# Optimization experiments

Hardware: AMD Instinct MI355X
Metric: run time of the kernel (lower is better)

Reference implementation:

```python
import jax, jax.numpy as jnp
import numpy as np

B, D, H = 32768, 688, 4
DH = D // H          # 172 head dim (d_model // h, overrides ctor d_k)
MH = 128             # mlp hidden
EPS = 1e-5
SCALE = 1.0 / float(np.sqrt(DH))


def _ln(x, g, b):
    m = jnp.mean(x, -1, keepdims=True)
    v = jnp.var(x, -1, keepdims=True)  # biased var, matches torch LayerNorm
    return (x - m) / jnp.sqrt(v + EPS) * g + b


def setup_inputs() -> dict:
    key = jax.random.key(0)
    ks = jax.random.split(key, 16)
    w = lambda k, o, i: jax.random.normal(k, (o, i), jnp.float32) * 0.001  # init.normal_(std=0.001)
    z = lambda n: jnp.zeros((n,), jnp.float32)
    o = lambda n: jnp.ones((n,), jnp.float32)
    return dict(
        x=jax.random.normal(ks[0], (B, D), jnp.float32),
        x2=jax.random.normal(ks[1], (B, D), jnp.float32),
        Wq_v=w(ks[2], D, D), bq_v=z(D),
        Wk_v=w(ks[3], D, D), bk_v=z(D),
        Wv_v=w(ks[4], D, D), bv_v=z(D),
        Wq_i=w(ks[5], D, D), bq_i=z(D),
        Wk_i=w(ks[6], D, D), bk_i=z(D),
        Wv_i=w(ks[7], D, D), bv_i=z(D),
        Wo_v=w(ks[8], D, D), bo_v=z(D),
        Wo_i=w(ks[9], D, D), bo_i=z(D),
        ln1_g=o(D), ln1_b=z(D), ln2_g=o(D), ln2_b=z(D),
        ln3_g=o(D), ln3_b=z(D), ln4_g=o(D), ln4_b=z(D),
        m1v_W=w(ks[10], MH, D), m1v_b=z(MH),
        m2v_W=w(ks[11], D, MH), m2v_b=z(D),
        m1i_W=w(ks[12], MH, D), m1i_b=z(MH),
        m2i_W=w(ks[13], D, MH), m2i_b=z(D),
        coef=o(8),  # LearnableCoefficient 1..8, all init to 1.0
    )


def reference(x, x2,
              Wq_v, bq_v, Wk_v, bk_v, Wv_v, bv_v,
              Wq_i, bq_i, Wk_i, bk_i, Wv_i, bv_i,
              Wo_v, bo_v, Wo_i, bo_i,
              ln1_g, ln1_b, ln2_g, ln2_b, ln3_g, ln3_b, ln4_g, ln4_b,
              m1v_W, m1v_b, m2v_W, m2v_b, m1i_W, m1i_b, m2i_W, m2i_b,
              coef):
    rgb = _ln(x, ln1_g, ln1_b)
    ir = _ln(x2, ln2_g, ln2_b)
    proj = lambda t, W, b: (t @ W.T + b).reshape(-1, H, DH)  # (B, h, d_k)
    q_vis, k_vis, v_vis = proj(rgb, Wq_v, bq_v), proj(rgb, Wk_v, bk_v), proj(rgb, Wv_v, bv_v)
    q_ir, k_ir, v_ir = proj(ir, Wq_i, bq_i), proj(ir, Wk_i, bk_i), proj(ir, Wv_i, bv_i)
    # cross attention over heads: scores are (B, h, h)
    att_vis = jax.nn.softmax(jnp.einsum('bhd,bgd->bhg', q_ir, k_vis) * SCALE, -1)
    att_ir = jax.nn.softmax(jnp.einsum('bhd,bgd->bhg', q_vis, k_ir) * SCALE, -1)
    out_vis = jnp.einsum('bhg,bgd->bhd', att_vis, v_vis).reshape(-1, D) @ Wo_v.T + bo_v
    out_ir = jnp.einsum('bhg,bgd->bhd', att_ir, v_ir).reshape(-1, D) @ Wo_i.T + bo_i
    out_vis = coef[0] * x + coef[1] * out_vis
    out_ir = coef[2] * x2 + coef[3] * out_ir
    mv = jax.nn.gelu(_ln(out_vis, ln3_g, ln3_b) @ m1v_W.T + m1v_b, approximate=False) @ m2v_W.T + m2v_b
    mi = jax.nn.gelu(_ln(out_ir, ln4_g, ln4_b) @ m1i_W.T + m1i_b, approximate=False) @ m2i_W.T + m2i_b
    out_vis = coef[4] * out_vis + coef[5] * mv
    out_ir = coef[6] * out_ir + coef[7] * mi
    return out_vis, out_ir
```

## Files before the change

kernel.cpp:

```cpp
#include <hip/hip_runtime.h>
#include <cmath>


#define B_ROWS 32768
#define D_DIM  688
#define DP     704
#define DH_DIM 172
#define MH_DIM 128

typedef unsigned short ushort_t;
typedef __attribute__((ext_vector_type(8))) __bf16 bf16x8;
typedef __attribute__((ext_vector_type(4))) float  f32x4;

__device__ __forceinline__ float b2f(ushort_t u) {
    return __builtin_bit_cast(float, (unsigned int)u << 16);
}
__device__ __forceinline__ ushort_t f2bf(float f) {
    unsigned int u = __builtin_bit_cast(unsigned int, f);
    u += 0x7FFFu + ((u >> 16) & 1u);
    return (ushort_t)(u >> 16);
}

__device__ __forceinline__ void gl2lds16(const ushort_t* g, ushort_t* l) {
    __builtin_amdgcn_global_load_lds(
        (const __attribute__((address_space(1))) unsigned int*)g,
        (__attribute__((address_space(3))) unsigned int*)l, 16, 0, 0);
}

struct CvtJobs {
    const float* src[12];
    ushort_t*    dst[12];
    int O[12], Opad[12], Kin[12], Kpad[12];
    int bstart[13];
};

__global__ __launch_bounds__(256)
void cvt_all(CvtJobs jobs)
{
    int b = blockIdx.x;
    int j = 0;
    while (b >= jobs.bstart[j + 1]) ++j;
    const int t = (b - jobs.bstart[j]) * 256 + threadIdx.x;
    const int Kpad = jobs.Kpad[j];
    const int Kin  = jobs.Kin[j];
    const int cpr  = Kpad >> 3;
    if (t >= jobs.Opad[j] * cpr) return;
    const int o = t / cpr;
    const int c = t - o * cpr;
    unsigned int p0 = 0, p1 = 0, p2 = 0, p3 = 0;
    if (o < jobs.O[j] && (c * 8 + 8) <= Kin) {
        const float* s = jobs.src[j] + (size_t)o * Kin + c * 8;
        float4 f0 = reinterpret_cast<const float4*>(s)[0];
        float4 f1 = reinterpret_cast<const float4*>(s)[1];
        p0 = f2bf(f0.x) | ((unsigned int)f2bf(f0.y) << 16);
        p1 = f2bf(f0.z) | ((unsigned int)f2bf(f0.w) << 16);
        p2 = f2bf(f1.x) | ((unsigned int)f2bf(f1.y) << 16);
        p3 = f2bf(f1.z) | ((unsigned int)f2bf(f1.w) << 16);
    }
    *reinterpret_cast<uint4*>(jobs.dst[j] + (size_t)o * Kpad + c * 8) =
        make_uint4(p0, p1, p2, p3);
}

__global__ __launch_bounds__(256)
void pack_bias(const float* __restrict__ a0, const float* __restrict__ a1,
               const float* __restrict__ a2, const float* __restrict__ b0,
               const float* __restrict__ b1, const float* __restrict__ b2,
               float* __restrict__ dv, float* __restrict__ di)
{
    int t = blockIdx.x * 256 + threadIdx.x;
    if (t >= 2064) return;
    float v, w;
    if (t < 688)       { v = a0[t];        w = b0[t]; }
    else if (t < 1376) { v = a1[t - 688];  w = b1[t - 688]; }
    else               { v = a2[t - 1376]; w = b2[t - 1376]; }
    dv[t] = v; di[t] = w;
}

__global__ __launch_bounds__(256)
void ln_kernel(const float* __restrict__ Xv, const float* __restrict__ Xi,
               const float* __restrict__ gv, const float* __restrict__ bv,
               const float* __restrict__ gi, const float* __restrict__ bi,
               ushort_t* __restrict__ Yv, ushort_t* __restrict__ Yi)
{
    const int lane = threadIdx.x & 63;
    const int wave = threadIdx.x >> 6;
    const long w = (long)blockIdx.x * 4 + wave;
    const float* X; const float* g; const float* b; ushort_t* Y; long r;
    if (w < B_ROWS) { X = Xv; g = gv; b = bv; Y = Yv; r = w; }
    else            { X = Xi; g = gi; b = bi; Y = Yi; r = w - B_ROWS; }

    const float4* row = reinterpret_cast<const float4*>(X + r * D_DIM);
    float4 v0 = row[lane];
    float4 v1 = row[lane + 64];
    float4 v2 = make_float4(0.f, 0.f, 0.f, 0.f);
    if (lane < 44) v2 = row[lane + 128];

    float s  = v0.x + v0.y + v0.z + v0.w + v1.x + v1.y + v1.z + v1.w
             + v2.x + v2.y + v2.z + v2.w;
    float s2 = v0.x*v0.x + v0.y*v0.y + v0.z*v0.z + v0.w*v0.w
             + v1.x*v1.x + v1.y*v1.y + v1.z*v1.z + v1.w*v1.w
             + v2.x*v2.x + v2.y*v2.y + v2.z*v2.z + v2.w*v2.w;
#pragma unroll
    for (int m = 32; m; m >>= 1) { s += __shfl_xor(s, m); s2 += __shfl_xor(s2, m); }

    const float mean = s * (1.f / 688.f);
    const float var  = s2 * (1.f / 688.f) - mean * mean;
    const float rstd = rsqrtf(var + 1e-5f);

    const float4* g4 = reinterpret_cast<const float4*>(g);
    const float4* b4 = reinterpret_cast<const float4*>(b);
    ushort4* out4 = reinterpret_cast<ushort4*>(Y + r * DP);

    {
        float4 gg = g4[lane], bb = b4[lane];
        ushort4 o;
        o.x = f2bf((v0.x - mean) * rstd * gg.x + bb.x);
        o.y = f2bf((v0.y - mean) * rstd * gg.y + bb.y);
        o.z = f2bf((v0.z - mean) * rstd * gg.z + bb.z);
        o.w = f2bf((v0.w - mean) * rstd * gg.w + bb.w);
        out4[lane] = o;
    }
    {
        float4 gg = g4[lane + 64], bb = b4[lane + 64];
        ushort4 o;
        o.x = f2bf((v1.x - mean) * rstd * gg.x + bb.x);
        o.y = f2bf((v1.y - mean) * rstd * gg.y + bb.y);
        o.z = f2bf((v1.z - mean) * rstd * gg.z + bb.z);
        o.w = f2bf((v1.w - mean) * rstd * gg.w + bb.w);
        out4[lane + 64] = o;
    }
    if (lane < 44) {
        float4 gg = g4[lane + 128], bb = b4[lane + 128];
        ushort4 o;
        o.x = f2bf((v2.x - mean) * rstd * gg.x + bb.x);
        o.y = f2bf((v2.y - mean) * rstd * gg.y + bb.y);
        o.z = f2bf((v2.z - mean) * rstd * gg.z + bb.z);
        o.w = f2bf((v2.w - mean) * rstd * gg.w + bb.w);
        out4[lane + 128] = o;
    } else if (lane < 48) {
        out4[lane + 128] = make_ushort4(0, 0, 0, 0);
    }
}

template<int MODE>
__global__ __launch_bounds__(512, 1)
void gemm8(const ushort_t* __restrict__ A0, const ushort_t* __restrict__ A1,
           const ushort_t* __restrict__ W0, const ushort_t* __restrict__ W1,
           const float* __restrict__ bias0, const float* __restrict__ bias1,
           ushort_t* __restrict__ out0, ushort_t* __restrict__ out1,
           const float* __restrict__ res0, const float* __restrict__ res1,
           const float* __restrict__ coef, int ca0, int cb0, int ca1, int cb1,
           int NBn, int N, int K, int lda, int ldw, int ldo)
{
    __shared__ __align__(16) ushort_t lds8[65536];

    const int q8 = gridDim.x >> 3;
    const int v  = (blockIdx.x & 7) * q8 + (blockIdx.x >> 3);
    const int nb = v % NBn;
    const int tmp = v / NBn;
    const int mb = tmp & 127;
    const int zz = tmp >> 7;

    const ushort_t* A = zz ? A1 : A0;
    const ushort_t* W = zz ? W1 : W0;
    const float* bias = zz ? bias1 : bias0;
    ushort_t* outp    = zz ? out1 : out0;
    const float* resid = zz ? res1 : res0;
    const int ca = zz ? ca1 : ca0;
    const int cb = zz ? cb1 : cb0;

    const int tid  = threadIdx.x;
    const int lane = tid & 63;
    const int wave = tid >> 6;
    const int wrow = wave >> 2;
    const int wcol = wave & 3;
    const int m0 = mb * 256;
    const int n0 = nb * 256;
    const int rl16 = lane & 15;
    const int q4   = lane >> 4;

    const int r0 = tid >> 3;
    const int u0 = tid & 7;
    const int swz0 = ((u0 ^ (r0 & 7)) * 8);

    f32x4 acc[8][4];
#pragma unroll
    for (int i = 0; i < 8; ++i)
#pragma unroll
        for (int j = 0; j < 4; ++j)
            acc[i][j] = f32x4{0.f, 0.f, 0.f, 0.f};

    const int NT = K >> 6;

#define STAGE8(mat, rbase, ld, kt, hf, tilebase) do {                              \
    const ushort_t* _s = (mat) + (size_t)((rbase) + (hf)*128 + r0) * (ld)          \
                         + (kt)*64 + swz0;                                         \
    gl2lds16(_s,                 (tilebase) + (hf)*8192 + wave*512);               \
    gl2lds16(_s + 64*(size_t)(ld), (tilebase) + (hf)*8192 + 4096 + wave*512);      \
} while (0)

#define RD_A(base, mib, kkv) do {                                                  \
    _Pragma("unroll")                                                              \
    for (int i = 0; i < 4; ++i) {                                                  \
        const int row_ = wrow*128 + ((mib)+i)*16 + rl16;                           \
        const int un_  = (((kkv) >> 3) + q4) ^ (lane & 7);                         \
        af[i] = *reinterpret_cast<const bf16x8*>((base) + row_*64 + un_*8);        \
    } } while (0)

#define RD_B(base, kkv) do {                                                       \
    _Pragma("unroll")                                                              \
    for (int j = 0; j < 4; ++j) {                                                  \
        const int row_ = wcol*64 + j*16 + rl16;                                    \
        const int un_  = (((kkv) >> 3) + q4) ^ (lane & 7);                         \
        bw[j] = *reinterpret_cast<const bf16x8*>((base) + row_*64 + un_*8);        \
    } } while (0)

#define MFMA16(mib) do {                                                           \
    __builtin_amdgcn_s_setprio(1);                                                 \
    _Pragma("unroll")                                                              \
    for (int i = 0; i < 4; ++i)                                                    \
    _Pragma("unroll")                                                              \
    for (int j = 0; j < 4; ++j)                                                    \
        acc[(mib)+i][j] =                                                          \
            __builtin_amdgcn_mfma_f32_16x16x32_bf16(af[i], bw[j], acc[(mib)+i][j], \
                                                    0, 0, 0);                      \
    __builtin_amdgcn_s_setprio(0);                                                 \
} while (0)

    STAGE8(A, m0, lda, 0, 0, lds8);
    STAGE8(A, m0, lda, 0, 1, lds8);
    STAGE8(W, n0, ldw, 0, 0, lds8 + 32768);
    STAGE8(W, n0, ldw, 0, 1, lds8 + 32768);
    STAGE8(W, n0, ldw, 1, 0, lds8 + 49152);
    asm volatile("s_waitcnt vmcnt(2)" ::: "memory");
    __builtin_amdgcn_s_barrier();

    for (int t = 0; t < NT; ++t) {
        ushort_t* const Ab  = lds8 + ((t & 1) * 16384);
        ushort_t* const Bb  = lds8 + 32768 + ((t & 1) * 16384);
        ushort_t* const An  = lds8 + (((t + 1) & 1) * 16384);
        ushort_t* const Bn1 = lds8 + 32768 + (((t + 1) & 1) * 16384);
        ushort_t* const Bn2 = Bb;
        const int tn1 = (t + 1 < NT) ? t + 1 : NT - 1;
        const int tn2 = (t + 2 < NT) ? t + 2 : NT - 1;

        bf16x8 af[4], bw[4];

        RD_A(Ab, 0, 0);
        RD_B(Bb, 0);
        STAGE8(A, m0, lda, tn1, 0, An);
        STAGE8(W, n0, ldw, tn1, 1, Bn1);
        __builtin_amdgcn_s_barrier();
        MFMA16(0);
        __builtin_amdgcn_s_barrier();

        RD_A(Ab, 4, 0);
        STAGE8(A, m0, lda, tn1, 1, An);
        __builtin_amdgcn_s_barrier();
        MFMA16(4);
        __builtin_amdgcn_s_barrier();

        RD_A(Ab, 0, 32);
        RD_B(Bb, 32);
        __builtin_amdgcn_s_barrier();
        MFMA16(0);
        __builtin_amdgcn_s_barrier();

        RD_A(Ab, 4, 32);
        STAGE8(W, n0, ldw, tn2, 0, Bn2);
        asm volatile("s_waitcnt vmcnt(2)" ::: "memory");
        __builtin_amdgcn_s_barrier();
        MFMA16(4);
        __builtin_amdgcn_s_barrier();
    }

    asm volatile("s_waitcnt vmcnt(0)" ::: "memory");
    __builtin_amdgcn_s_barrier();

    ushort_t* const Cl = lds8;
#pragma unroll
    for (int mi = 0; mi < 8; ++mi)
#pragma unroll
        for (int nj = 0; nj < 4; ++nj)
#pragma unroll
            for (int r = 0; r < 4; ++r) {
                const int row  = wrow*128 + mi*16 + q4*4 + r;
                const int colL = wcol*64 + nj*16 + rl16;
                const int blk  = (colL >> 3) ^ (((row >> 2) & 3) << 1);
                Cl[row*256 + blk*8 + (colL & 7)] = f2bf(acc[mi][nj][r]);
            }
    __syncthreads();

    float cA = 0.f, cB = 1.f;
    if constexpr (MODE == 1) { cA = coef[ca]; cB = coef[cb]; }
#pragma unroll
    for (int it2 = 0; it2 < 16; ++it2) {
        const int c   = it2 * 512 + tid;
        const int row = c >> 5;
        const int lb  = c & 31;
        const int gcol = n0 + lb * 8;
        if (gcol >= N) continue;
        const int pb = lb ^ (((row >> 2) & 3) << 1);
        uint4 pv = *reinterpret_cast<const uint4*>(Cl + row*256 + pb*8);
        const ushort_t* pu = (const ushort_t*)&pv;
        float4 b0 = *reinterpret_cast<const float4*>(bias + gcol);
        float4 b1 = *reinterpret_cast<const float4*>(bias + gcol + 4);
        const float bb[8] = {b0.x, b0.y, b0.z, b0.w, b1.x, b1.y, b1.z, b1.w};
        const size_t idx = (size_t)(m0 + row) * ldo + gcol;
        ushort_t o[8];
        if constexpr (MODE == 0) {
#pragma unroll
            for (int k = 0; k < 8; ++k) o[k] = f2bf(b2f(pu[k]) + bb[k]);
        } else {
            const float* rp = resid + idx;
            float4 r0_ = reinterpret_cast<const float4*>(rp)[0];
            float4 r1_ = reinterpret_cast<const float4*>(rp)[1];
            const float rr[8] = {r0_.x, r0_.y, r0_.z, r0_.w, r1_.x, r1_.y, r1_.z, r1_.w};
#pragma unroll
            for (int k = 0; k < 8; ++k)
                o[k] = f2bf(cA * rr[k] + cB * (b2f(pu[k]) + bb[k]));
        }
        *reinterpret_cast<uint4*>(outp + idx) = *reinterpret_cast<uint4*>(o);
    }
#undef STAGE8
#undef RD_A
#undef RD_B
#undef MFMA16
}

__global__ __launch_bounds__(256)
void mlp_fused(const ushort_t* __restrict__ ov0, const ushort_t* __restrict__ ov1,
               const float* __restrict__ g0, const float* __restrict__ b0,
               const float* __restrict__ g1, const float* __restrict__ b1,
               const ushort_t* __restrict__ W10, const ushort_t* __restrict__ W11,
               const float* __restrict__ mb10, const float* __restrict__ mb11,
               const ushort_t* __restrict__ W20, const ushort_t* __restrict__ W21,
               const float* __restrict__ mb20, const float* __restrict__ mb21,
               const float* __restrict__ coef,
               float* __restrict__ out0, float* __restrict__ out1)
{
    __shared__ __align__(16) ushort_t hraw[32 * 712];
    __shared__ __align__(16) ushort_t gbuf[32 * 136];
    __shared__ float glds[704];
    __shared__ float blds[704];
    __shared__ float mlds[32];
    __shared__ float rlds[32];

    const int zz = blockIdx.y;
    const ushort_t* ovb = zz ? ov1 : ov0;
    const float* lg = zz ? g1 : g0;
    const float* lb = zz ? b1 : b0;
    const ushort_t* W1 = zz ? W11 : W10;
    const float* mb1 = zz ? mb11 : mb10;
    const ushort_t* W2 = zz ? W21 : W20;
    const float* mb2 = zz ? mb21 : mb20;
    float* outp = zz ? out1 : out0;
    const float cA = coef[zz ? 6 : 4];
    const float cB = coef[zz ? 7 : 5];

    const int tid  = threadIdx.x;
    const int lane = tid & 63;
    const int wv   = tid >> 6;
    const long r0  = (long)blockIdx.x * 32;

    if (tid < 176) {
        float4 gg = make_float4(0, 0, 0, 0), bb = make_float4(0, 0, 0, 0);
        if (tid < 172) {
            gg = reinterpret_cast<const float4*>(lg)[tid];
            bb = reinterpret_cast<const float4*>(lb)[tid];
        }
        reinterpret_cast<float4*>(glds)[tid] = gg;
        reinterpret_cast<float4*>(blds)[tid] = bb;
    }

#pragma unroll
    for (int it = 0; it < 11; ++it) {
        const int c = it * 256 + tid;
        const int row = c / 88;
        const int u = c - row * 88;
        uint4 vv = make_uint4(0, 0, 0, 0);
        if (u < 86)
            vv = *reinterpret_cast<const uint4*>(ovb + (r0 + row) * 688 + u * 8);
        *reinterpret_cast<uint4*>(&hraw[row * 712 + u * 8]) = vv;
    }
    __syncthreads();

    for (int rr = 0; rr < 8; ++rr) {
        const int row = wv * 8 + rr;
        const ushort_t* hp = &hraw[row * 712];
        ushort4 a0 = *reinterpret_cast<const ushort4*>(hp + lane * 4);
        ushort4 a1 = *reinterpret_cast<const ushort4*>(hp + 256 + lane * 4);
        ushort4 a2 = make_ushort4(0, 0, 0, 0);
        if (lane < 44) a2 = *reinterpret_cast<const ushort4*>(hp + 512 + lane * 4);
        float e[12] = {b2f(a0.x), b2f(a0.y), b2f(a0.z), b2f(a0.w),
                       b2f(a1.x), b2f(a1.y), b2f(a1.z), b2f(a1.w),
                       b2f(a2.x), b2f(a2.y), b2f(a2.z), b2f(a2.w)};
        float s = 0.f, s2 = 0.f;
#pragma unroll
        for (int k = 0; k < 12; ++k) { s += e[k]; s2 += e[k] * e[k]; }
#pragma unroll
        for (int m = 32; m; m >>= 1) { s += __shfl_xor(s, m); s2 += __shfl_xor(s2, m); }
        if (lane == 0) {
            const float mean = s * (1.f / 688.f);
            const float var  = s2 * (1.f / 688.f) - mean * mean;
            mlds[row] = mean;
            rlds[row] = rsqrtf(var + 1e-5f);
        }
    }
    __syncthreads();

#pragma unroll
    for (int it = 0; it < 11; ++it) {
        const int c = it * 256 + tid;
        if (c < 2752) {
            const int row = c / 86;
            const int u = c - row * 86;
            uint4 vv = *reinterpret_cast<const uint4*>(&hraw[row * 712 + u * 8]);
            const float mean = mlds[row], rstd = rlds[row];
            const ushort_t* pe = (const ushort_t*)&vv;
            ushort_t o[8];
#pragma unroll
            for (int k = 0; k < 8; ++k)
                o[k] = f2bf((b2f(pe[k]) - mean) * rstd * glds[u * 8 + k] + blds[u * 8 + k]);
            *reinterpret_cast<uint4*>(&hraw[row * 712 + u * 8]) = *reinterpret_cast<uint4*>(o);
        }
    }
    __syncthreads();

    const int rl16 = lane & 15;
    const int q4   = lane >> 4;

    {
        f32x4 acc[2][2];
#pragma unroll
        for (int i = 0; i < 2; ++i) { acc[i][0] = f32x4{0,0,0,0}; acc[i][1] = f32x4{0,0,0,0}; }
        for (int kt = 0; kt < 11; ++kt) {
#pragma unroll
            for (int kk = 0; kk < 64; kk += 32) {
                bf16x8 af[2], bw[2];
#pragma unroll
                for (int n = 0; n < 2; ++n)
                    bw[n] = *reinterpret_cast<const bf16x8*>(
                        W1 + (size_t)(wv * 32 + n * 16 + rl16) * 704 + kt * 64 + kk + q4 * 8);
#pragma unroll
                for (int i = 0; i < 2; ++i)
                    af[i] = *reinterpret_cast<const bf16x8*>(
                        &hraw[(i * 16 + rl16) * 712 + kt * 64 + kk + q4 * 8]);
#pragma unroll
                for (int i = 0; i < 2; ++i)
#pragma unroll
                    for (int n = 0; n < 2; ++n)
                        acc[i][n] = __builtin_amdgcn_mfma_f32_16x16x32_bf16(
                            af[i], bw[n], acc[i][n], 0, 0, 0);
            }
        }
        const int rb = q4 * 4;
#pragma unroll
        for (int n = 0; n < 2; ++n) {
            const int col = wv * 32 + n * 16 + rl16;
            const float bc = mb1[col];
#pragma unroll
            for (int i = 0; i < 2; ++i)
#pragma unroll
                for (int r = 0; r < 4; ++r) {
                    float val = acc[i][n][r] + bc;
                    val = 0.5f * val * (1.0f + erff(val * 0.70710678118654752f));
                    gbuf[(i * 16 + rb + r) * 136 + col] = f2bf(val);
                }
        }
    }
    __syncthreads();

    for (int ch = 0; ch < 11; ++ch) {
        const int col16 = wv * 176 + ch * 16;
        if (col16 >= 688) continue;
        f32x4 acc2[2];
        acc2[0] = f32x4{0, 0, 0, 0};
        acc2[1] = f32x4{0, 0, 0, 0};
#pragma unroll
        for (int kk = 0; kk < 4; ++kk) {
            bf16x8 bw2 = *reinterpret_cast<const bf16x8*>(
                W2 + (size_t)(col16 + rl16) * 128 + kk * 32 + q4 * 8);
            bf16x8 af2[2];
#pragma unroll
            for (int i = 0; i < 2; ++i)
                af2[i] = *reinterpret_cast<const bf16x8*>(
                    &gbuf[(i * 16 + rl16) * 136 + kk * 32 + q4 * 8]);
#pragma unroll
            for (int i = 0; i < 2; ++i)
                acc2[i] = __builtin_amdgcn_mfma_f32_16x16x32_bf16(af2[i], bw2, acc2[i], 0, 0, 0);
        }
        const int col = col16 + rl16;
        const float bc = mb2[col];
#pragma unroll
        for (int i = 0; i < 2; ++i)
#pragma unroll
            for (int r = 0; r < 4; ++r) {
                const long row = r0 + i * 16 + q4 * 4 + r;
                const float raw = b2f(ovb[row * 688 + col]);
                outp[row * 688 + col] = cA * raw + cB * (acc2[i][r] + bc);
            }
    }
}

__global__ __launch_bounds__(256)
void attn_kernel(const ushort_t* __restrict__ qkv_v, const ushort_t* __restrict__ qkv_i,
                 ushort_t* __restrict__ ctx_v, ushort_t* __restrict__ ctx_i)
{
    const int lane = threadIdx.x & 63;
    const int wave = threadIdx.x >> 6;
    const long r = (long)blockIdx.x * 4 + wave;
    const ushort_t* bv = qkv_v + r * 2064;
    const ushort_t* bi = qkv_i + r * 2064;

    float sv[4][4], si[4][4];
#pragma unroll
    for (int h = 0; h < 4; ++h)
#pragma unroll
        for (int g = 0; g < 4; ++g) { sv[h][g] = 0.f; si[h][g] = 0.f; }

    float vvr[3][4], vir[3][4];
#pragma unroll
    for (int it = 0; it < 3; ++it) {
        const int d = lane + it * 64;
        const bool ok = d < DH_DIM;
        float qv[4], kv[4], qi[4], ki[4];
#pragma unroll
        for (int h = 0; h < 4; ++h) {
            const int o = h * DH_DIM + d;
            qv[h]      = ok ? b2f(bv[o]) : 0.f;
            kv[h]      = ok ? b2f(bv[D_DIM + o]) : 0.f;
            vvr[it][h] = ok ? b2f(bv[2 * D_DIM + o]) : 0.f;
            qi[h]      = ok ? b2f(bi[o]) : 0.f;
            ki[h]      = ok ? b2f(bi[D_DIM + o]) : 0.f;
            vir[it][h] = ok ? b2f(bi[2 * D_DIM + o]) : 0.f;
        }
#pragma unroll
        for (int h = 0; h < 4; ++h)
#pragma unroll
            for (int g = 0; g < 4; ++g) {
                sv[h][g] += qi[h] * kv[g];
                si[h][g] += qv[h] * ki[g];
            }
    }

#pragma unroll
    for (int h = 0; h < 4; ++h)
#pragma unroll
        for (int g = 0; g < 4; ++g) {
            float a = sv[h][g], b = si[h][g];
#pragma unroll
            for (int m = 32; m; m >>= 1) { a += __shfl_xor(a, m); b += __shfl_xor(b, m); }
            sv[h][g] = a; si[h][g] = b;
        }

    const float scale = 0.07624928516630235f;
    float av[4][4], ai[4][4];
#pragma unroll
    for (int h = 0; h < 4; ++h) {
        float m1 = fmaxf(fmaxf(sv[h][0], sv[h][1]), fmaxf(sv[h][2], sv[h][3])) * scale;
        float m2 = fmaxf(fmaxf(si[h][0], si[h][1]), fmaxf(si[h][2], si[h][3])) * scale;
        float d1 = 0.f, d2 = 0.f;
#pragma unroll
        for (int g = 0; g < 4; ++g) {
            av[h][g] = expf(sv[h][g] * scale - m1); d1 += av[h][g];
            ai[h][g] = expf(si[h][g] * scale - m2); d2 += ai[h][g];
        }
        const float r1 = 1.f / d1, r2 = 1.f / d2;
#pragma unroll
        for (int g = 0; g < 4; ++g) { av[h][g] *= r1; ai[h][g] *= r2; }
    }

#pragma unroll
    for (int it = 0; it < 3; ++it) {
        const int d = lane + it * 64;
        if (d < DH_DIM) {
#pragma unroll
            for (int h = 0; h < 4; ++h) {
                float cv = av[h][0] * vvr[it][0] + av[h][1] * vvr[it][1]
                         + av[h][2] * vvr[it][2] + av[h][3] * vvr[it][3];
                float ci = ai[h][0] * vir[it][0] + ai[h][1] * vir[it][1]
                         + ai[h][2] * vir[it][2] + ai[h][3] * vir[it][3];
                ctx_v[r * DP + h * DH_DIM + d] = f2bf(cv);
                ctx_i[r * DP + h * DH_DIM + d] = f2bf(ci);
            }
        }
    }
    if (lane < 16) {
        ctx_v[r * DP + 688 + lane] = 0;
        ctx_i[r * DP + 688 + lane] = 0;
    }
}

extern "C" void kernel_launch(void* const* d_in, const int* in_sizes, int n_in,
                              void* d_out, int out_size, void* d_ws, size_t ws_size,
                              hipStream_t stream)
{
    if (n_in < 35) return;
    const float* x     = (const float*)d_in[0];
    const float* x2    = (const float*)d_in[1];
    const float* Wq_v  = (const float*)d_in[2];
    const float* bq_v  = (const float*)d_in[3];
    const float* Wk_v  = (const float*)d_in[4];
    const float* bk_v  = (const float*)d_in[5];
    const float* Wv_v  = (const float*)d_in[6];
    const float* bv_v  = (const float*)d_in[7];
    const float* Wq_i  = (const float*)d_in[8];
    const float* bq_i  = (const float*)d_in[9];
    const float* Wk_i  = (const float*)d_in[10];
    const float* bk_i  = (const float*)d_in[11];
    const float* Wv_i  = (const float*)d_in[12];
    const float* bv_i  = (const float*)d_in[13];
    const float* Wo_v  = (const float*)d_in[14];
    const float* bo_v  = (const float*)d_in[15];
    const float* Wo_i  = (const float*)d_in[16];
    const float* bo_i  = (const float*)d_in[17];
    const float* ln1_g = (const float*)d_in[18];
    const float* ln1_b = (const float*)d_in[19];
    const float* ln2_g = (const float*)d_in[20];
    const float* ln2_b = (const float*)d_in[21];
    const float* ln3_g = (const float*)d_in[22];
    const float* ln3_b = (const float*)d_in[23];
    const float* ln4_g = (const float*)d_in[24];
    const float* ln4_b = (const float*)d_in[25];
    const float* m1v_W = (const float*)d_in[26];
    const float* m1v_b = (const float*)d_in[27];
    const float* m2v_W = (const float*)d_in[28];
    const float* m2v_b = (const float*)d_in[29];
    const float* m1i_W = (const float*)d_in[30];
    const float* m1i_b = (const float*)d_in[31];
    const float* m2i_W = (const float*)d_in[32];
    const float* m2i_b = (const float*)d_in[33];
    const float* coef  = (const float*)d_in[34];

    const size_t BDP = (size_t)B_ROWS * DP;
    const size_t BD  = (size_t)B_ROWS * D_DIM;

    char* ws = (char*)d_ws;
    size_t off = 0;
    auto give = [&](size_t bytes) {
        char* p = ws + off;
        off += (bytes + 255) & ~(size_t)255;
        return p;
    };
    ushort_t* Wcat_v = (ushort_t*)give(2304ull * DP * 2);
    ushort_t* Wcat_i = (ushort_t*)give(2304ull * DP * 2);
    ushort_t* Wo_vb  = (ushort_t*)give(768ull * DP * 2);
    ushort_t* Wo_ib  = (ushort_t*)give(768ull * DP * 2);
    ushort_t* m1vb   = (ushort_t*)give(128ull * DP * 2);
    ushort_t* m1ib   = (ushort_t*)give(128ull * DP * 2);
    ushort_t* m2vb   = (ushort_t*)give(768ull * 128 * 2);
    ushort_t* m2ib   = (ushort_t*)give(768ull * 128 * 2);
    float*    bcat_v = (float*)give(2064 * 4);
    float*    bcat_i = (float*)give(2064 * 4);
    char* regX = give(BDP * 2 * 2);
    char* regQ = give((size_t)B_ROWS * 2064 * 2 * 2);
    if (ws_size < off) return;

    ushort_t* xn_v  = (ushort_t*)regX;
    ushort_t* xn_i  = xn_v + BDP;
    ushort_t* ctx_v = xn_v;
    ushort_t* ctx_i = xn_i;
    ushort_t* qkv_v = (ushort_t*)regQ;
    ushort_t* qkv_i = qkv_v + (size_t)B_ROWS * 2064;
    ushort_t* ovb   = (ushort_t*)regQ;
    ushort_t* oib   = ovb + BD;

    float* ov = (float*)d_out;
    float* oi = ov + BD;

    CvtJobs J;
    const float* srcs[12] = {Wq_v, Wk_v, Wv_v, Wq_i, Wk_i, Wv_i,
                             Wo_v, Wo_i, m1v_W, m1i_W, m2v_W, m2i_W};
    ushort_t* dsts[12] = {Wcat_v, Wcat_v + 688 * DP, Wcat_v + 1376 * DP,
                          Wcat_i, Wcat_i + 688 * DP, Wcat_i + 1376 * DP,
                          Wo_vb, Wo_ib, m1vb, m1ib, m2vb, m2ib};
    int Os[12]    = {688, 688, 688, 688, 688, 688, 688, 688, 128, 128, 688, 688};
    int Opads[12] = {688, 688, 928, 688, 688, 928, 768, 768, 128, 128, 768, 768};
    int Kins[12]  = {688, 688, 688, 688, 688, 688, 688, 688, 688, 688, 128, 128};
    int Kpads[12] = {DP, DP, DP, DP, DP, DP, DP, DP, DP, DP, 128, 128};
    int bs = 0;
    for (int j = 0; j < 12; ++j) {
        J.src[j] = srcs[j]; J.dst[j] = dsts[j];
        J.O[j] = Os[j]; J.Opad[j] = Opads[j]; J.Kin[j] = Kins[j]; J.Kpad[j] = Kpads[j];
        J.bstart[j] = bs;
        bs += (Opads[j] * (Kpads[j] >> 3) + 255) / 256;
    }
    J.bstart[12] = bs;
    cvt_all<<<dim3(bs), dim3(256), 0, stream>>>(J);

    pack_bias<<<dim3(9), dim3(256), 0, stream>>>(bq_v, bk_v, bv_v, bq_i, bk_i, bv_i,
                                                 bcat_v, bcat_i);

    ln_kernel<<<dim3(2 * B_ROWS / 4), dim3(256), 0, stream>>>(
        x, x2, ln1_g, ln1_b, ln2_g, ln2_b, xn_v, xn_i);

    gemm8<0><<<dim3(128 * 9 * 2), dim3(512), 0, stream>>>(
        xn_v, xn_i, Wcat_v, Wcat_i, bcat_v, bcat_i, qkv_v, qkv_i,
        nullptr, nullptr, nullptr, 0, 0, 0, 0, 9, 2064, DP, DP, DP, 2064);

    attn_kernel<<<dim3(B_ROWS / 4), dim3(256), 0, stream>>>(qkv_v, qkv_i, ctx_v, ctx_i);

    gemm8<1><<<dim3(128 * 3 * 2), dim3(512), 0, stream>>>(
        ctx_v, ctx_i, Wo_vb, Wo_ib, bo_v, bo_i, ovb, oib,
        x, x2, coef, 0, 1, 2, 3, 3, 688, DP, DP, DP, 688);

    mlp_fused<<<dim3(B_ROWS / 32, 2), dim3(256), 0, stream>>>(
        ovb, oib, ln3_g, ln3_b, ln4_g, ln4_b,
        m1vb, m1ib, m1v_b, m1i_b, m2vb, m2ib, m2v_b, m2i_b,
        coef, ov, oi);
}
```

Before: 681.6 us.

## Replace 256x256 GEMM tile with 256x128 tile and triple-buffered K=32 pipeline

Rewrites the projection GEMM kernel to use a 256x128 output tile with 8 waves in a 4x2 layout, a K step of 32, and a three-stage LDS ring (72 KB instead of 128 KB). This permits two blocks per CU. It also lowers weight padding from 928 to 800 rows, which cuts wasted N tiles on the QKV GEMM. The aim is better occupancy and less padding waste, at the cost of lower arithmetic intensity per tile and more barriers per FLOP.

```diff
diff --git a/kernel.cpp b/kernel.cpp
--- a/kernel.cpp
+++ b/kernel.cpp
@@ -143,8 +143,8 @@
 }
 
 template<int MODE>
-__global__ __launch_bounds__(512, 1)
-void gemm8(const ushort_t* __restrict__ A0, const ushort_t* __restrict__ A1,
+__global__ __launch_bounds__(512, 2)
+void gemmT(const ushort_t* __restrict__ A0, const ushort_t* __restrict__ A1,
            const ushort_t* __restrict__ W0, const ushort_t* __restrict__ W1,
            const float* __restrict__ bias0, const float* __restrict__ bias1,
            ushort_t* __restrict__ out0, ushort_t* __restrict__ out1,
@@ -152,7 +152,7 @@
            const float* __restrict__ coef, int ca0, int cb0, int ca1, int cb1,
            int NBn, int N, int K, int lda, int ldw, int ldo)
 {
-    __shared__ __align__(16) ushort_t lds8[65536];
+    __shared__ __align__(16) ushort_t lds[36864];
 
     const int q8 = gridDim.x >> 3;
     const int v  = (blockIdx.x & 7) * q8 + (blockIdx.x >> 3);
@@ -172,136 +172,97 @@
     const int tid  = threadIdx.x;
     const int lane = tid & 63;
     const int wave = tid >> 6;
-    const int wrow = wave >> 2;
-    const int wcol = wave & 3;
+    const int wrow = wave >> 1;
+    const int wcol = wave & 1;
     const int m0 = mb * 256;
-    const int n0 = nb * 256;
+    const int n0 = nb * 128;
     const int rl16 = lane & 15;
     const int q4   = lane >> 4;
 
-    const int r0 = tid >> 3;
-    const int u0 = tid & 7;
-    const int swz0 = ((u0 ^ (r0 & 7)) * 8);
-
-    f32x4 acc[8][4];
-#pragma unroll
-    for (int i = 0; i < 8; ++i)
+    const int r0a  = tid >> 2;
+    const int swzk = ((tid & 3) ^ ((tid >> 3) & 3)) * 8;
+
+    f32x4 acc[4][4];
+#pragma unroll
+    for (int i = 0; i < 4; ++i)
 #pragma unroll
         for (int j = 0; j < 4; ++j)
             acc[i][j] = f32x4{0.f, 0.f, 0.f, 0.f};
 
-    const int NT = K >> 6;
-
-#define STAGE8(mat, rbase, ld, kt, hf, tilebase) do {                              \
-    const ushort_t* _s = (mat) + (size_t)((rbase) + (hf)*128 + r0) * (ld)          \
-                         + (kt)*64 + swz0;                                         \
-    gl2lds16(_s,                 (tilebase) + (hf)*8192 + wave*512);               \
-    gl2lds16(_s + 64*(size_t)(ld), (tilebase) + (hf)*8192 + 4096 + wave*512);      \
+    const int NT = K >> 5;
+
+#define STAGET(kt, bb) do {                                                        \
+    const ushort_t* _sa = A + (size_t)(m0 + r0a) * lda + (kt)*32 + swzk;           \
+    gl2lds16(_sa,                    lds + (bb)*12288 + wave*512);                 \
+    gl2lds16(_sa + 128*(size_t)lda,  lds + (bb)*12288 + 4096 + wave*512);          \
+    const ushort_t* _sb = W + (size_t)(n0 + r0a) * ldw + (kt)*32 + swzk;           \
+    gl2lds16(_sb,                    lds + (bb)*12288 + 8192 + wave*512);          \
 } while (0)
 
-#define RD_A(base, mib, kkv) do {                                                  \
-    _Pragma("unroll")                                                              \
-    for (int i = 0; i < 4; ++i) {                                                  \
-        const int row_ = wrow*128 + ((mib)+i)*16 + rl16;                           \
-        const int un_  = (((kkv) >> 3) + q4) ^ (lane & 7);                         \
-        af[i] = *reinterpret_cast<const bf16x8*>((base) + row_*64 + un_*8);        \
-    } } while (0)
-
-#define RD_B(base, kkv) do {                                                       \
-    _Pragma("unroll")                                                              \
-    for (int j = 0; j < 4; ++j) {                                                  \
-        const int row_ = wcol*64 + j*16 + rl16;                                    \
-        const int un_  = (((kkv) >> 3) + q4) ^ (lane & 7);                         \
-        bw[j] = *reinterpret_cast<const bf16x8*>((base) + row_*64 + un_*8);        \
-    } } while (0)
-
-#define MFMA16(mib) do {                                                           \
-    __builtin_amdgcn_s_setprio(1);                                                 \
-    _Pragma("unroll")                                                              \
-    for (int i = 0; i < 4; ++i)                                                    \
-    _Pragma("unroll")                                                              \
-    for (int j = 0; j < 4; ++j)                                                    \
-        acc[(mib)+i][j] =                                                          \
-            __builtin_amdgcn_mfma_f32_16x16x32_bf16(af[i], bw[j], acc[(mib)+i][j], \
-                                                    0, 0, 0);                      \
-    __builtin_amdgcn_s_setprio(0);                                                 \
-} while (0)
-
-    STAGE8(A, m0, lda, 0, 0, lds8);
-    STAGE8(A, m0, lda, 0, 1, lds8);
-    STAGE8(W, n0, ldw, 0, 0, lds8 + 32768);
-    STAGE8(W, n0, ldw, 0, 1, lds8 + 32768);
-    STAGE8(W, n0, ldw, 1, 0, lds8 + 49152);
-    asm volatile("s_waitcnt vmcnt(2)" ::: "memory");
+    STAGET(0, 0);
+    STAGET(1, 1);
+    asm volatile("s_waitcnt vmcnt(3)" ::: "memory");
     __builtin_amdgcn_s_barrier();
 
     for (int t = 0; t < NT; ++t) {
-        ushort_t* const Ab  = lds8 + ((t & 1) * 16384);
-        ushort_t* const Bb  = lds8 + 32768 + ((t & 1) * 16384);
-        ushort_t* const An  = lds8 + (((t + 1) & 1) * 16384);
-        ushort_t* const Bn1 = lds8 + 32768 + (((t + 1) & 1) * 16384);
-        ushort_t* const Bn2 = Bb;
-        const int tn1 = (t + 1 < NT) ? t + 1 : NT - 1;
+        const int cbuf = t % 3;
+        const int pbuf = (t + 2) % 3;
         const int tn2 = (t + 2 < NT) ? t + 2 : NT - 1;
 
         bf16x8 af[4], bw[4];
-
-        RD_A(Ab, 0, 0);
-        RD_B(Bb, 0);
-        STAGE8(A, m0, lda, tn1, 0, An);
-        STAGE8(W, n0, ldw, tn1, 1, Bn1);
+#pragma unroll
+        for (int i = 0; i < 4; ++i) {
+            const int row_ = wrow * 64 + i * 16 + rl16;
+            af[i] = *reinterpret_cast<const bf16x8*>(
+                lds + cbuf * 12288 + row_ * 32 + ((q4 ^ ((row_ >> 1) & 3)) * 8));
+        }
+#pragma unroll
+        for (int j = 0; j < 4; ++j) {
+            const int row_ = wcol * 64 + j * 16 + rl16;
+            bw[j] = *reinterpret_cast<const bf16x8*>(
+                lds + cbuf * 12288 + 8192 + row_ * 32 + ((q4 ^ ((row_ >> 1) & 3)) * 8));
+        }
+        STAGET(tn2, pbuf);
+        asm volatile("s_waitcnt vmcnt(3)" ::: "memory");
         __builtin_amdgcn_s_barrier();
-        MFMA16(0);
-        __builtin_amdgcn_s_barrier();
-
-        RD_A(Ab, 4, 0);
-        STAGE8(A, m0, lda, tn1, 1, An);
-        __builtin_amdgcn_s_barrier();
-        MFMA16(4);
-        __builtin_amdgcn_s_barrier();
-
-        RD_A(Ab, 0, 32);
-        RD_B(Bb, 32);
-        __builtin_amdgcn_s_barrier();
-        MFMA16(0);
-        __builtin_amdgcn_s_barrier();
-
-        RD_A(Ab, 4, 32);
-        STAGE8(W, n0, ldw, tn2, 0, Bn2);
-        asm volatile("s_waitcnt vmcnt(2)" ::: "memory");
-        __builtin_amdgcn_s_barrier();
-        MFMA16(4);
+        __builtin_amdgcn_s_setprio(1);
+#pragma unroll
+        for (int i = 0; i < 4; ++i)
+#pragma unroll
+            for (int j = 0; j < 4; ++j)
+                acc[i][j] = __builtin_amdgcn_mfma_f32_16x16x32_bf16(af[i], bw[j], acc[i][j], 0, 0, 0);
+        __builtin_amdgcn_s_setprio(0);
         __builtin_amdgcn_s_barrier();
     }
 
     asm volatile("s_waitcnt vmcnt(0)" ::: "memory");
     __builtin_amdgcn_s_barrier();
 
-    ushort_t* const Cl = lds8;
-#pragma unroll
-    for (int mi = 0; mi < 8; ++mi)
+    ushort_t* const Cl = lds;
+#pragma unroll
+    for (int mi = 0; mi < 4; ++mi)
 #pragma unroll
         for (int nj = 0; nj < 4; ++nj)
 #pragma unroll
             for (int r = 0; r < 4; ++r) {
-                const int row  = wrow*128 + mi*16 + q4*4 + r;
-                const int colL = wcol*64 + nj*16 + rl16;
+                const int row  = wrow * 64 + mi * 16 + q4 * 4 + r;
+                const int colL = wcol * 64 + nj * 16 + rl16;
                 const int blk  = (colL >> 3) ^ (((row >> 2) & 3) << 1);
-                Cl[row*256 + blk*8 + (colL & 7)] = f2bf(acc[mi][nj][r]);
+                Cl[row * 128 + blk * 8 + (colL & 7)] = f2bf(acc[mi][nj][r]);
             }
     __syncthreads();
 
     float cA = 0.f, cB = 1.f;
     if constexpr (MODE == 1) { cA = coef[ca]; cB = coef[cb]; }
 #pragma unroll
-    for (int it2 = 0; it2 < 16; ++it2) {
+    for (int it2 = 0; it2 < 8; ++it2) {
         const int c   = it2 * 512 + tid;
-        const int row = c >> 5;
-        const int lb  = c & 31;
+        const int row = c >> 4;
+        const int lb  = c & 15;
         const int gcol = n0 + lb * 8;
         if (gcol >= N) continue;
         const int pb = lb ^ (((row >> 2) & 3) << 1);
-        uint4 pv = *reinterpret_cast<const uint4*>(Cl + row*256 + pb*8);
+        uint4 pv = *reinterpret_cast<const uint4*>(Cl + row * 128 + pb * 8);
         const ushort_t* pu = (const ushort_t*)&pv;
         float4 b0 = *reinterpret_cast<const float4*>(bias + gcol);
         float4 b1 = *reinterpret_cast<const float4*>(bias + gcol + 4);
@@ -322,10 +283,7 @@
         }
         *reinterpret_cast<uint4*>(outp + idx) = *reinterpret_cast<uint4*>(o);
     }
-#undef STAGE8
-#undef RD_A
-#undef RD_B
-#undef MFMA16
+#undef STAGET
 }
 
 __global__ __launch_bounds__(256)
@@ -676,7 +634,7 @@
                           Wcat_i, Wcat_i + 688 * DP, Wcat_i + 1376 * DP,
                           Wo_vb, Wo_ib, m1vb, m1ib, m2vb, m2ib};
     int Os[12]    = {688, 688, 688, 688, 688, 688, 688, 688, 128, 128, 688, 688};
-    int Opads[12] = {688, 688, 928, 688, 688, 928, 768, 768, 128, 128, 768, 768};
+    int Opads[12] = {688, 688, 800, 688, 688, 800, 768, 768, 128, 128, 768, 768};
     int Kins[12]  = {688, 688, 688, 688, 688, 688, 688, 688, 688, 688, 128, 128};
     int Kpads[12] = {DP, DP, DP, DP, DP, DP, DP, DP, DP, DP, 128, 128};
     int bs = 0;
@@ -695,15 +653,15 @@
     ln_kernel<<<dim3(2 * B_ROWS / 4), dim3(256), 0, stream>>>(
         x, x2, ln1_g, ln1_b, ln2_g, ln2_b, xn_v, xn_i);
 
-    gemm8<0><<<dim3(128 * 9 * 2), dim3(512), 0, stream>>>(
+    gemmT<0><<<dim3(128 * 17 * 2), dim3(512), 0, stream>>>(
         xn_v, xn_i, Wcat_v, Wcat_i, bcat_v, bcat_i, qkv_v, qkv_i,
-        nullptr, nullptr, nullptr, 0, 0, 0, 0, 9, 2064, DP, DP, DP, 2064);
+        nullptr, nullptr, nullptr, 0, 0, 0, 0, 17, 2064, DP, DP, DP, 2064);
 
     attn_kernel<<<dim3(B_ROWS / 4), dim3(256), 0, stream>>>(qkv_v, qkv_i, ctx_v, ctx_i);
 
-    gemm8<1><<<dim3(128 * 3 * 2), dim3(512), 0, stream>>>(
+    gemmT<1><<<dim3(128 * 6 * 2), dim3(512), 0, stream>>>(
         ctx_v, ctx_i, Wo_vb, Wo_ib, bo_v, bo_i, ovb, oib,
-        x, x2, coef, 0, 1, 2, 3, 3, 688, DP, DP, DP, 688);
+        x, x2, coef, 0, 1, 2, 3, 6, 688, DP, DP, DP, 688);
 
     mlp_fused<<<dim3(B_ROWS / 32, 2), dim3(256), 0, stream>>>(
         ovb, oib, ln3_g, ln3_b, ln4_g, ln4_b,
```

Measured after the change: 689.7 us. Within noise of the previous version (+1.2%).
